# Performance work log

Hardware: AMD Instinct MI355X
Metric: run time of the kernel (lower is better)

The kernel has to match this reference:

```python
import jax, jax.numpy as jnp
import numpy as np
from jax.scipy.linalg import cholesky, solve_triangular

EPS = 0.001

def setup_inputs() -> dict:
    key = jax.random.key(0)
    k1, = jax.random.split(key, 1)
    b, w, h, c = 64, 56, 56, 256
    x = jax.random.normal(k1, (b, w, h, c), dtype=jnp.float32)
    gamma = jnp.ones((c,), dtype=jnp.float32)
    beta = jnp.zeros((c,), dtype=jnp.float32)
    return {"x": x, "gamma": gamma, "beta": beta}

def reference(x, gamma, beta):
    b, w, h, c = x.shape
    n = b * w * h
    # (c, b*w*h) layout as in the original transpose(3,0,1,2)+reshape
    x_flat = jnp.transpose(x, (3, 0, 1, 2)).reshape(c, n)
    m = jnp.mean(x_flat, axis=1, keepdims=True)           # (c, 1)
    f = x_flat - m                                        # (c, n)
    ff = (f @ f.T) / (jnp.float32(n) - 1.0)               # (c, c) covariance
    ff = (1.0 - EPS) * ff + EPS * jnp.eye(c, dtype=x.dtype)
    L = cholesky(ff, lower=True)
    inv_sqrt = solve_triangular(L, jnp.eye(c, dtype=x.dtype), lower=True)  # L^{-1}
    f_hat = inv_sqrt @ f                                  # (c, n) whitened
    out = jnp.transpose(f_hat.reshape(c, b, w, h), (1, 2, 3, 0))
    out = out * gamma.reshape(1, 1, 1, c) + beta.reshape(1, 1, 1, c)
    return out
```

## Files before the change

### kernel.cpp

```cpp
#include <hip/hip_runtime.h>
#include <hip/hip_bf16.h>
#include <math.h>

#define C 256
#define NROWS (64*56*56)
#define EPSV 0.001f
#define TRI(i) (((i)*((i)+1))>>1)

typedef __attribute__((ext_vector_type(8))) short bf16x8;
typedef __attribute__((ext_vector_type(4))) float f32x4;
typedef __attribute__((ext_vector_type(4))) unsigned short u16x4;
typedef __attribute__((ext_vector_type(8))) unsigned short u16x8;
#define MFMA16 __builtin_amdgcn_mfma_f32_16x16x32_bf16

__device__ __forceinline__ int PAD(int i) {
    int a = i >> 2, b = i & 3;
    return ((a + 1) * (2 * a + b)) << 2;
}

__device__ __forceinline__ float bcastf(float v, int l) {
    return __int_as_float(__builtin_amdgcn_readlane(__float_as_int(v), l));
}

__device__ __forceinline__ void split2(float v0, float v1, unsigned& hi, unsigned& lo) {
    unsigned b0 = __float_as_uint(v0), b1 = __float_as_uint(v1);
    hi = (b0 >> 16) | (b1 & 0xFFFF0000u);
    float l0 = v0 - __uint_as_float(b0 & 0xFFFF0000u);
    float l1 = v1 - __uint_as_float(b1 & 0xFFFF0000u);
    lo = (__float_as_uint(l0) >> 16) | (__float_as_uint(l1) & 0xFFFF0000u);
}


template<int W>
__device__ __forceinline__ void cov_step(f32x4* acc, const unsigned* lh, const unsigned* ll,
                                         int m, int kg) {
    constexpr int R0 = W, R1 = 15 - W;
    constexpr int O1 = W + 1;
    bf16x8 ah[2], al[2];
    {
        int r0 = R0 * 16 + m, r1 = R1 * 16 + m;
        int o0 = r0 * 20 + ((kg ^ ((r0 >> 3) & 3)) << 2);
        int o1 = r1 * 20 + ((kg ^ ((r1 >> 3) & 3)) << 2);
        ah[0] = *(const bf16x8*)&lh[o0]; al[0] = *(const bf16x8*)&ll[o0];
        ah[1] = *(const bf16x8*)&lh[o1]; al[1] = *(const bf16x8*)&ll[o1];
    }
#pragma unroll
    for (int c = 0; c <= R1; ++c) {
        int rb = c * 16 + m;
        int ob = rb * 20 + ((kg ^ ((rb >> 3) & 3)) << 2);
        bf16x8 bh = *(const bf16x8*)&lh[ob];
        bf16x8 bl = *(const bf16x8*)&ll[ob];
        if (c <= R0) {
            acc[c] = MFMA16(ah[0], bh, acc[c], 0, 0, 0);
            acc[c] = MFMA16(ah[0], bl, acc[c], 0, 0, 0);
            acc[c] = MFMA16(al[0], bh, acc[c], 0, 0, 0);
        }
        {
            acc[O1 + c] = MFMA16(ah[1], bh, acc[O1 + c], 0, 0, 0);
            acc[O1 + c] = MFMA16(ah[1], bl, acc[O1 + c], 0, 0, 0);
            acc[O1 + c] = MFMA16(al[1], bh, acc[O1 + c], 0, 0, 0);
        }
    }
}

template<int W>
__device__ __forceinline__ void cov_out(const f32x4* acc, float* Sc, int m, int kg) {
    constexpr int R[2] = {W, 15 - W};
    constexpr int O[2] = {0, W + 1};
#pragma unroll
    for (int rr = 0; rr < 2; ++rr) {
        int i0 = R[rr] * 16 + kg * 4;
#pragma unroll
        for (int c = 0; c < 16; ++c) {
            if (c <= R[rr]) {
                int j = c * 16 + m;
#pragma unroll
                for (int q = 0; q < 4; ++q)
                    atomicAdd(&Sc[(i0 + q) * 256 + j], acc[O[rr] + c][q]);
            }
        }
    }
}

__global__ __launch_bounds__(512, 4) void k_cov(const float* __restrict__ x,
                                                float* __restrict__ S8,
                                                float* __restrict__ sums) {
    __shared__ unsigned lh[256 * 20];
    __shared__ unsigned ll_[256 * 20];
    int tid = threadIdx.x, wave = tid >> 6, lane = tid & 63;
    int m = lane & 15, kg = lane >> 4;
    int ch = tid & 255, half = tid >> 8;
    const float* xc = x + (size_t)blockIdx.x * 448 * 256 + ch;
    f32x4 acc[17];
#pragma unroll
    for (int t = 0; t < 17; ++t) acc[t] = 0.f;
    float colsum = 0.f;
    int swkey = (ch >> 3) & 3;

    for (int it = 0; it < 14; ++it) {
        __syncthreads();
        const float* xr = xc + it * 32 * 256;
#pragma unroll
        for (int j = 0; j < 8; ++j) {
            int rp = half * 8 + j;
            float v0 = xr[(2 * rp) * 256];
            float v1 = xr[(2 * rp + 1) * 256];
            colsum += v0 + v1;
            unsigned h, l;
            split2(v0, v1, h, l);
            int idx = ch * 20 + ((((rp >> 2) ^ swkey) << 2) | (rp & 3));
            lh[idx] = h;
            ll_[idx] = l;
        }
        __syncthreads();
        switch (wave) {
            case 0: cov_step<0>(acc, lh, ll_, m, kg); break;
            case 1: cov_step<1>(acc, lh, ll_, m, kg); break;
            case 2: cov_step<2>(acc, lh, ll_, m, kg); break;
            case 3: cov_step<3>(acc, lh, ll_, m, kg); break;
            case 4: cov_step<4>(acc, lh, ll_, m, kg); break;
            case 5: cov_step<5>(acc, lh, ll_, m, kg); break;
            case 6: cov_step<6>(acc, lh, ll_, m, kg); break;
            default: cov_step<7>(acc, lh, ll_, m, kg); break;
        }
    }
    atomicAdd(&sums[ch], colsum);
    float* Sc = S8 + (size_t)(blockIdx.x & 7) * 65536;
    switch (wave) {
        case 0: cov_out<0>(acc, Sc, m, kg); break;
        case 1: cov_out<1>(acc, Sc, m, kg); break;
        case 2: cov_out<2>(acc, Sc, m, kg); break;
        case 3: cov_out<3>(acc, Sc, m, kg); break;
        case 4: cov_out<4>(acc, Sc, m, kg); break;
        case 5: cov_out<5>(acc, Sc, m, kg); break;
        case 6: cov_out<6>(acc, Sc, m, kg); break;
        default: cov_out<7>(acc, Sc, m, kg); break;
    }
}

__global__ __launch_bounds__(256) void k_init(const float* __restrict__ S8,
                                              const float* __restrict__ sums,
                                              float* __restrict__ Lg) {
    int u = blockIdx.x * 256 + threadIdx.x;
    int i = u >> 6, j0 = (u & 63) << 2;
    if (j0 > i) return;
    const float scale = (1.f - EPSV) / ((float)NROWS - 1.f);
    f32x4 s4 = 0.f;
#pragma unroll
    for (int p = 0; p < 8; ++p)
        s4 += *(const f32x4*)&S8[p * 65536 + i * C + j0];
    float mi = sums[i] * (1.f / (float)NROWS);
    f32x4 mj = *(const f32x4*)&sums[j0];
    int base = PAD(i);
#pragma unroll
    for (int e = 0; e < 4; ++e) {
        int j = j0 + e;
        if (j <= i) {
            float v = (s4[e] - mi * mj[e]) * scale;
            if (j == i) v += EPSV;
            Lg[base + j] = v;
        }
    }
}

__global__ __launch_bounds__(512) void k_panel(float* __restrict__ Lg, int kb) {
    __shared__ __align__(16) float DS[32 * 36];
    int tid = threadIdx.x;
    int lane = tid & 63;
    int k0 = kb * 32;

    if (tid < 64) {
        int col = lane & 31;
        float a[32];
#pragma unroll
        for (int i = 0; i < 32; ++i) {
            int ii = (i >= col) ? i : col;
            int jj = (i >= col) ? col : i;
            a[i] = Lg[PAD(k0 + ii) + k0 + jj];
        }
        float drec = 0.f;
#pragma unroll
        for (int k = 0; k < 32; ++k) {
            float akk = bcastf(a[k], k);
            float rinv = rsqrtf(akk);
            float myl = a[k] * rinv;
            bool up = (col > k);
#pragma unroll
            for (int i = k + 1; i < 32; ++i) {
                float lik = bcastf(a[i], k) * rinv;
                if (up) a[i] -= lik * myl;
                if (col == k) a[i] = lik;
            }
            if (col == k) { a[k] = akk * rinv; drec = rinv; }
        }
        float xv[32];
#pragma unroll
        for (int i = 0; i < 32; ++i) xv[i] = (col == i) ? 1.f : 0.f;
#pragma unroll
        for (int i = 0; i < 32; ++i) {
            float di = bcastf(drec, i);
            float xi = xv[i] * di;
            xv[i] = xi;
#pragma unroll
            for (int j = i + 1; j < 32; ++j) {
                float lji = bcastf(a[j], i);
                xv[j] -= lji * xi;
            }
        }
        if (lane < 32) {
#pragma unroll
            for (int i = 0; i < 32; ++i) {
                DS[i * 36 + col] = xv[i];
                if (i >= col) Lg[PAD(k0 + i) + k0 + col] = xv[i];
            }
        }
    }
    __syncthreads();

    int m = 224 - k0;
    int r = tid >> 1, g = tid & 1;
    if (r < m) {
        int abase = PAD(k0 + 32 + r) + k0;
        float4 av[8];
#pragma unroll
        for (int q = 0; q < 8; ++q) av[q] = *(const float4*)&Lg[abase + q * 4];
#pragma unroll
        for (int tgrp = 0; tgrp < 4; ++tgrp) {
            int cbase = g * 16 + tgrp * 4;
            float rv[4];
#pragma unroll
            for (int cc = 0; cc < 4; ++cc) {
                const float* drow = &DS[(cbase + cc) * 36];
                float s = 0.f;
#pragma unroll
                for (int q = 0; q < 8; ++q) {
                    float4 d4 = *(const float4*)&drow[q * 4];
                    s += av[q].x*d4.x + av[q].y*d4.y + av[q].z*d4.z + av[q].w*d4.w;
                }
                rv[cc] = s;
            }
            float4 res; res.x = rv[0]; res.y = rv[1]; res.z = rv[2]; res.w = rv[3];
            *(float4*)&Lg[abase + cbase] = res;
        }
    }
}

__global__ __launch_bounds__(256) void k_trail(float* __restrict__ Lg, int kb) {
    __shared__ __align__(16) float As[32][36];
    __shared__ __align__(16) float Bs[32][36];
    int tid = threadIdx.x;
    int p = blockIdx.x;
    int a2 = 0;
    while (TRI(a2 + 1) <= p) ++a2;
    int b2 = p - TRI(a2);
    int ib2 = kb + 1 + a2, jb2 = kb + 1 + b2;
    int k0 = kb * 32;

    {
        int r = tid >> 3, cq = (tid & 7) * 4;
        *(float4*)&As[r][cq] = *(const float4*)&Lg[PAD(ib2 * 32 + r) + k0 + cq];
        *(float4*)&Bs[r][cq] = *(const float4*)&Lg[PAD(jb2 * 32 + r) + k0 + cq];
    }
    __syncthreads();

    int r2 = (tid >> 4) * 2, c2 = (tid & 15) * 2;
    float t00 = 0, t01 = 0, t10 = 0, t11 = 0;
#pragma unroll 8
    for (int q = 0; q < 32; ++q) {
        float a0 = As[r2][q], a1 = As[r2 + 1][q];
        float b0 = Bs[c2][q], b1 = Bs[c2 + 1][q];
        t00 += a0 * b0; t01 += a0 * b1;
        t10 += a1 * b0; t11 += a1 * b1;
    }
    int gi = ib2 * 32 + r2, gj = jb2 * 32 + c2;
    if (ib2 != jb2) {
        float* p0 = &Lg[PAD(gi) + gj];
        float* p1 = &Lg[PAD(gi + 1) + gj];
        p0[0] -= t00; p0[1] -= t01;
        p1[0] -= t10; p1[1] -= t11;
    } else {
        if (c2     <= r2    ) Lg[PAD(gi) + gj]         -= t00;
        if (c2 + 1 <= r2    ) Lg[PAD(gi) + gj + 1]     -= t01;
        if (c2     <= r2 + 1) Lg[PAD(gi + 1) + gj]     -= t10;
        if (c2 + 1 <= r2 + 1) Lg[PAD(gi + 1) + gj + 1] -= t11;
    }
}

__global__ __launch_bounds__(256) void k_inv(const float* __restrict__ Lg,
                                             const float* __restrict__ sums,
                                             const float* __restrict__ gamma,
                                             unsigned short* __restrict__ Wphi,
                                             unsigned short* __restrict__ Wplo,
                                             float* __restrict__ biasacc) {
    __shared__ __align__(16) float Wcol[256][36];
    __shared__ __align__(16) float Ls[32][36];
    __shared__ __align__(16) float Tst[32][36];
    int jbb = blockIdx.x;
    int tid = threadIdx.x;
    int j0 = jbb * 32;

    {
        int r = tid >> 3, cq = (tid & 7) * 4;
        const float* row = &Lg[PAD(j0 + r) + j0];
        float4 v;
        v.x = (cq     <= r) ? row[cq]     : 0.f;
        v.y = (cq + 1 <= r) ? row[cq + 1] : 0.f;
        v.z = (cq + 2 <= r) ? row[cq + 2] : 0.f;
        v.w = (cq + 3 <= r) ? row[cq + 3] : 0.f;
        *(float4*)&Wcol[j0 + r][cq] = v;
    }
    __syncthreads();

    int r2 = (tid >> 4) * 2, c2 = (tid & 15) * 2;
    for (int ib = jbb + 1; ib < 8; ++ib) {
        int i0 = ib * 32;
        float t00 = 0, t01 = 0, t10 = 0, t11 = 0;
        for (int kb = jbb; kb < ib; ++kb) {
            __syncthreads();
            {
                int r = tid >> 3, cq = (tid & 7) * 4;
                *(float4*)&Ls[r][cq] = *(const float4*)&Lg[PAD(i0 + r) + kb * 32 + cq];
            }
            __syncthreads();
            int kw = kb * 32;
#pragma unroll 8
            for (int q = 0; q < 32; ++q) {
                float l0 = Ls[r2][q], l1 = Ls[r2 + 1][q];
                float w0 = Wcol[kw + q][c2], w1 = Wcol[kw + q][c2 + 1];
                t00 += l0 * w0; t01 += l0 * w1;
                t10 += l1 * w0; t11 += l1 * w1;
            }
        }
        __syncthreads();
        Tst[r2][c2] = t00;     Tst[r2][c2 + 1] = t01;
        Tst[r2 + 1][c2] = t10; Tst[r2 + 1][c2 + 1] = t11;
        {
            int r = tid >> 3, cq = (tid & 7) * 4;
            const float* row = &Lg[PAD(i0 + r) + i0];
            float4 v;
            v.x = (cq     <= r) ? row[cq]     : 0.f;
            v.y = (cq + 1 <= r) ? row[cq + 1] : 0.f;
            v.z = (cq + 2 <= r) ? row[cq + 2] : 0.f;
            v.w = (cq + 3 <= r) ? row[cq + 3] : 0.f;
            *(float4*)&Ls[r][cq] = v;
        }
        __syncthreads();
        float w00 = 0, w01 = 0, w10 = 0, w11 = 0;
#pragma unroll 8
        for (int q = 0; q < 32; ++q) {
            float d0 = Ls[r2][q], d1 = Ls[r2 + 1][q];
            float tq0 = Tst[q][c2], tq1 = Tst[q][c2 + 1];
            w00 += d0 * tq0; w01 += d0 * tq1;
            w10 += d1 * tq0; w11 += d1 * tq1;
        }
        Wcol[i0 + r2][c2] = -w00;     Wcol[i0 + r2][c2 + 1] = -w01;
        Wcol[i0 + r2 + 1][c2] = -w10; Wcol[i0 + r2 + 1][c2 + 1] = -w11;
    }
    __syncthreads();

    {
        int r = tid;
        if (r >= j0) {
            float s = 0.f;
#pragma unroll 8
            for (int c = 0; c < 32; ++c)
                s += Wcol[r][c] * sums[j0 + c];
            atomicAdd(&biasacc[r], s * (1.f / (float)NROWS));
        }
    }
    for (int pi = tid; pi < 1024; pi += 256) {
        int jt = pi >> 6, l = pi & 63;
        int row = jt * 16 + (l & 15);
        int cb = (l >> 4) * 8;
        float g = (row >= j0) ? gamma[row] : 0.f;
        u16x4 h0, h1, lo0, lo1;
#pragma unroll
        for (int j = 0; j < 8; ++j) {
            float v = (row >= j0) ? g * Wcol[row][cb + j] : 0.f;
            unsigned b = __float_as_uint(v);
            unsigned short hi = (unsigned short)(b >> 16);
            float lf = v - __uint_as_float(b & 0xFFFF0000u);
            unsigned short lo = (unsigned short)(__float_as_uint(lf) >> 16);
            if (j < 4) { h0[j] = hi; lo0[j] = lo; }
            else       { h1[j - 4] = hi; lo1[j - 4] = lo; }
        }
        size_t base = ((size_t)(jt * 8 + jbb) * 64 + l) * 8;
        *(u16x4*)&Wphi[base]     = h0;
        *(u16x4*)&Wphi[base + 4] = h1;
        *(u16x4*)&Wplo[base]     = lo0;
        *(u16x4*)&Wplo[base + 4] = lo1;
    }
}

__global__ __launch_bounds__(512) void k_apply(const float* __restrict__ x,
                                               const unsigned short* __restrict__ Wphi,
                                               const unsigned short* __restrict__ Wplo,
                                               const float* __restrict__ beta,
                                               const float* __restrict__ gamma,
                                               const float* __restrict__ biasacc,
                                               float* __restrict__ out) {
    __shared__ unsigned short Bh[8192];
    __shared__ unsigned short Bl[8192];
    int tid = threadIdx.x, wave = tid >> 6, lane = tid & 63;
    int m = lane & 15, kg = lane >> 4;
    size_t rbase = (size_t)blockIdx.x * 128 + wave * 16;
    const float* xr = x + (rbase + m) * 256;

    f32x4 acc[16];
#pragma unroll
    for (int t = 0; t < 16; ++t) acc[t] = 0.f;

#pragma unroll
    for (int kcg = 0; kcg < 8; ++kcg) {
        __syncthreads();
#pragma unroll
        for (int v = tid; v < 1024; v += 512) {
            int jt = v >> 6, off = (v & 63) * 8;
            size_t src = (size_t)(jt * 8 + kcg) * 512 + off;
            int dst = jt * 512 + off;
            *(u16x8*)&Bh[dst] = *(const u16x8*)&Wphi[src];
            *(u16x8*)&Bl[dst] = *(const u16x8*)&Wplo[src];
        }
        f32x4 a0 = *(const f32x4*)&xr[kcg * 32 + kg * 8];
        f32x4 a1 = *(const f32x4*)&xr[kcg * 32 + kg * 8 + 4];
        bf16x8 ah;
#pragma unroll
        for (int e = 0; e < 4; ++e) {
            unsigned b0 = __float_as_uint(a0[e]);
            b0 += 0x7FFFu + ((b0 >> 16) & 1u);
            ah[e] = (short)(b0 >> 16);
            unsigned b1 = __float_as_uint(a1[e]);
            b1 += 0x7FFFu + ((b1 >> 16) & 1u);
            ah[4 + e] = (short)(b1 >> 16);
        }
        __syncthreads();
#pragma unroll
        for (int jt = 0; jt < 16; ++jt) {
            bf16x8 bh = *(const bf16x8*)&Bh[jt * 512 + lane * 8];
            bf16x8 bl = *(const bf16x8*)&Bl[jt * 512 + lane * 8];
            acc[jt] = MFMA16(ah, bh, acc[jt], 0, 0, 0);
            acc[jt] = MFMA16(ah, bl, acc[jt], 0, 0, 0);
        }
    }

#pragma unroll
    for (int jt = 0; jt < 16; ++jt) {
        int j = jt * 16 + m;
        float bb = beta[j] - gamma[j] * biasacc[j];
#pragma unroll
        for (int q = 0; q < 4; ++q)
            out[(rbase + kg * 4 + q) * 256 + j] = acc[jt][q] + bb;
    }
}

extern "C" void kernel_launch(void* const* d_in, const int* in_sizes, int n_in,
                              void* d_out, int out_size, void* d_ws, size_t ws_size,
                              hipStream_t stream) {
    const float* x     = (const float*)d_in[0];
    const float* gamma = (const float*)d_in[1];
    const float* beta  = (const float*)d_in[2];
    float* out  = (float*)d_out;
    float* ws   = (float*)d_ws;
    float* sums     = ws;
    float* biasacc  = ws + 256;
    float* S8       = ws + 512;
    float* Lg       = ws + 524800;
    unsigned short* Wphi = (unsigned short*)(ws + 558080);
    unsigned short* Wplo = (unsigned short*)(ws + 590848);

    hipMemsetAsync(ws, 0, 524800 * sizeof(float), stream);
    hipLaunchKernelGGL(k_cov, dim3(448), dim3(512), 0, stream, x, S8, sums);
    hipLaunchKernelGGL(k_init, dim3(64), dim3(256), 0, stream, S8, sums, Lg);
    for (int kb = 0; kb < 8; ++kb) {
        hipLaunchKernelGGL(k_panel, dim3(1), dim3(512), 0, stream, Lg, kb);
        int np = TRI(7 - kb);
        if (np > 0)
            hipLaunchKernelGGL(k_trail, dim3(np), dim3(256), 0, stream, Lg, kb);
    }
    hipLaunchKernelGGL(k_inv, dim3(8), dim3(256), 0, stream, Lg, sums, gamma, Wphi, Wplo, biasacc);
    hipLaunchKernelGGL(k_apply, dim3(1568), dim3(512), 0, stream, x, Wphi, Wplo, beta, gamma, biasacc, out);
}
```

Measured before the change: 617.7 us.

## Replace atomic covariance reduction with partials and fuse Cholesky into one kernel

The covariance kernel now runs 224 blocks, each covering twice as many rows, and writes its per-wave MFMA accumulators as plain partial tiles instead of issuing atomicAdds into 8 replicated matrices. A new init kernel sums those partials per tile. The 16 separate panel and trailing-update launches are merged into a single-block k_fact kernel that holds the packed lower triangle in LDS for the whole factorization. This removes atomic contention, the large memset and launch overhead, at the cost of fewer cov blocks and a serialized single-workgroup factorization with many barriers.

```diff
diff --git a/kernel.cpp b/kernel.cpp
--- a/kernel.cpp
+++ b/kernel.cpp
@@ -6,6 +6,7 @@
 #define NROWS (64*56*56)
 #define EPSV 0.001f
 #define TRI(i) (((i)*((i)+1))>>1)
+#define NBLK 224
 
 typedef __attribute__((ext_vector_type(8))) short bf16x8;
 typedef __attribute__((ext_vector_type(4))) float f32x4;
@@ -16,10 +17,6 @@
 __device__ __forceinline__ int PAD(int i) {
     int a = i >> 2, b = i & 3;
     return ((a + 1) * (2 * a + b)) << 2;
-}
-
-__device__ __forceinline__ float bcastf(float v, int l) {
-    return __int_as_float(__builtin_amdgcn_readlane(__float_as_int(v), l));
 }
 
 __device__ __forceinline__ void split2(float v0, float v1, unsigned& hi, unsigned& lo) {
@@ -63,41 +60,22 @@
     }
 }
 
-template<int W>
-__device__ __forceinline__ void cov_out(const f32x4* acc, float* Sc, int m, int kg) {
-    constexpr int R[2] = {W, 15 - W};
-    constexpr int O[2] = {0, W + 1};
-#pragma unroll
-    for (int rr = 0; rr < 2; ++rr) {
-        int i0 = R[rr] * 16 + kg * 4;
-#pragma unroll
-        for (int c = 0; c < 16; ++c) {
-            if (c <= R[rr]) {
-                int j = c * 16 + m;
-#pragma unroll
-                for (int q = 0; q < 4; ++q)
-                    atomicAdd(&Sc[(i0 + q) * 256 + j], acc[O[rr] + c][q]);
-            }
-        }
-    }
-}
-
 __global__ __launch_bounds__(512, 4) void k_cov(const float* __restrict__ x,
-                                                float* __restrict__ S8,
+                                                float* __restrict__ P,
                                                 float* __restrict__ sums) {
     __shared__ unsigned lh[256 * 20];
     __shared__ unsigned ll_[256 * 20];
     int tid = threadIdx.x, wave = tid >> 6, lane = tid & 63;
     int m = lane & 15, kg = lane >> 4;
     int ch = tid & 255, half = tid >> 8;
-    const float* xc = x + (size_t)blockIdx.x * 448 * 256 + ch;
+    const float* xc = x + (size_t)blockIdx.x * 896 * 256 + ch;
     f32x4 acc[17];
 #pragma unroll
     for (int t = 0; t < 17; ++t) acc[t] = 0.f;
     float colsum = 0.f;
     int swkey = (ch >> 3) & 3;
 
-    for (int it = 0; it < 14; ++it) {
+    for (int it = 0; it < 28; ++it) {
         __syncthreads();
         const float* xr = xc + it * 32 * 256;
 #pragma unroll
@@ -125,165 +103,208 @@
         }
     }
     atomicAdd(&sums[ch], colsum);
-    float* Sc = S8 + (size_t)(blockIdx.x & 7) * 65536;
-    switch (wave) {
-        case 0: cov_out<0>(acc, Sc, m, kg); break;
-        case 1: cov_out<1>(acc, Sc, m, kg); break;
-        case 2: cov_out<2>(acc, Sc, m, kg); break;
-        case 3: cov_out<3>(acc, Sc, m, kg); break;
-        case 4: cov_out<4>(acc, Sc, m, kg); break;
-        case 5: cov_out<5>(acc, Sc, m, kg); break;
-        case 6: cov_out<6>(acc, Sc, m, kg); break;
-        default: cov_out<7>(acc, Sc, m, kg); break;
-    }
-}
-
-__global__ __launch_bounds__(256) void k_init(const float* __restrict__ S8,
+    float* Pb = P + ((size_t)(blockIdx.x * 8 + wave) * 17) * 256;
+#pragma unroll
+    for (int t = 0; t < 17; ++t)
+        *(f32x4*)&Pb[t * 256 + lane * 4] = acc[t];
+}
+
+__global__ __launch_bounds__(256) void k_init(const float* __restrict__ P,
                                               const float* __restrict__ sums,
                                               float* __restrict__ Lg) {
-    int u = blockIdx.x * 256 + threadIdx.x;
-    int i = u >> 6, j0 = (u & 63) << 2;
-    if (j0 > i) return;
+    int chunk = blockIdx.x;
+    int W = chunk / 17, t = chunk % 17;
+    int R  = (t <= W) ? W : 15 - W;
+    int tj = (t <= W) ? t : t - W - 1;
+    int tid = threadIdx.x;
+    int lane = tid >> 2, q = tid & 3;
+    int kg = lane >> 4, m = lane & 15;
+    int i = R * 16 + kg * 4 + q;
+    int j = tj * 16 + m;
+
+    float s = 0.f;
+    const float* p = P + (size_t)(W * 17 + t) * 256 + tid;
+#pragma unroll 4
+    for (int b = 0; b < NBLK; ++b)
+        s += p[(size_t)b * 8 * 17 * 256];
+
+    if (j > i) return;
     const float scale = (1.f - EPSV) / ((float)NROWS - 1.f);
-    f32x4 s4 = 0.f;
-#pragma unroll
-    for (int p = 0; p < 8; ++p)
-        s4 += *(const f32x4*)&S8[p * 65536 + i * C + j0];
-    float mi = sums[i] * (1.f / (float)NROWS);
-    f32x4 mj = *(const f32x4*)&sums[j0];
-    int base = PAD(i);
-#pragma unroll
-    for (int e = 0; e < 4; ++e) {
-        int j = j0 + e;
-        if (j <= i) {
-            float v = (s4[e] - mi * mj[e]) * scale;
-            if (j == i) v += EPSV;
-            Lg[base + j] = v;
-        }
-    }
-}
-
-__global__ __launch_bounds__(512) void k_panel(float* __restrict__ Lg, int kb) {
-    __shared__ __align__(16) float DS[32 * 36];
+    float v = (s - sums[i] * sums[j] * (1.f / (float)NROWS)) * scale;
+    if (i == j) v += EPSV;
+    Lg[PAD(i) + j] = v;
+}
+
+template<int NR>
+__device__ __forceinline__ void trail_unit(float* __restrict__ Lp, int k0,
+                                           int ib2, int jb2, int r4, int c4) {
+    int gj = jb2 * 32 + c4;
+    int brow[4], arow[NR];
+#pragma unroll
+    for (int cc = 0; cc < 4; ++cc) brow[cc] = PAD(gj + cc) + k0;
+#pragma unroll
+    for (int rr = 0; rr < NR; ++rr) arow[rr] = PAD(ib2 * 32 + r4 + rr) + k0;
+    float acc[NR][4];
+#pragma unroll
+    for (int rr = 0; rr < NR; ++rr)
+#pragma unroll
+        for (int cc = 0; cc < 4; ++cc) acc[rr][cc] = 0.f;
+#pragma unroll
+    for (int k4 = 0; k4 < 32; k4 += 4) {
+        float4 b0 = *(const float4*)&Lp[brow[0] + k4];
+        float4 b1 = *(const float4*)&Lp[brow[1] + k4];
+        float4 b2 = *(const float4*)&Lp[brow[2] + k4];
+        float4 b3 = *(const float4*)&Lp[brow[3] + k4];
+#pragma unroll
+        for (int rr = 0; rr < NR; ++rr) {
+            float4 av = *(const float4*)&Lp[arow[rr] + k4];
+            acc[rr][0] += av.x*b0.x + av.y*b0.y + av.z*b0.z + av.w*b0.w;
+            acc[rr][1] += av.x*b1.x + av.y*b1.y + av.z*b1.z + av.w*b1.w;
+            acc[rr][2] += av.x*b2.x + av.y*b2.y + av.z*b2.z + av.w*b2.w;
+            acc[rr][3] += av.x*b3.x + av.y*b3.y + av.z*b3.z + av.w*b3.w;
+        }
+    }
+    if (ib2 != jb2) {
+#pragma unroll
+        for (int rr = 0; rr < NR; ++rr) {
+            int wb = PAD(ib2 * 32 + r4 + rr) + gj;
+            float4 o = *(const float4*)&Lp[wb];
+            o.x -= acc[rr][0]; o.y -= acc[rr][1]; o.z -= acc[rr][2]; o.w -= acc[rr][3];
+            *(float4*)&Lp[wb] = o;
+        }
+    } else {
+#pragma unroll
+        for (int rr = 0; rr < NR; ++rr) {
+            int rloc = r4 + rr;
+            int wb = PAD(ib2 * 32 + rloc) + gj;
+#pragma unroll
+            for (int cc = 0; cc < 4; ++cc)
+                if (c4 + cc <= rloc) Lp[wb + cc] -= acc[rr][cc];
+        }
+    }
+}
+
+__global__ __launch_bounds__(512, 2) void k_fact(float* __restrict__ Lg) {
+    __shared__ __align__(16) float Lp[33280];
+    __shared__ __align__(16) float D0[1056];
+    __shared__ __align__(16) float DS[1152];
     int tid = threadIdx.x;
-    int lane = tid & 63;
-    int k0 = kb * 32;
-
-    if (tid < 64) {
-        int col = lane & 31;
-        float a[32];
-#pragma unroll
-        for (int i = 0; i < 32; ++i) {
-            int ii = (i >= col) ? i : col;
-            int jj = (i >= col) ? col : i;
-            a[i] = Lg[PAD(k0 + ii) + k0 + jj];
-        }
-        float drec = 0.f;
-#pragma unroll
+    int slot = tid >> 6, sub = tid & 63;
+    int c4 = (sub & 7) * 4;
+
+    for (int u = tid; u < 8320; u += 512)
+        *(f32x4*)&Lp[u * 4] = *(const f32x4*)&Lg[u * 4];
+
+    int ei0, ej0, ei1 = -1, ej1 = 0;
+    {
+        int e = tid;
+        int i = (int)((sqrtf(8.f * (float)e + 1.f) - 1.f) * 0.5f);
+        while (TRI(i) > e) --i;
+        while (TRI(i + 1) <= e) ++i;
+        ei0 = i; ej0 = e - TRI(i);
+        if (tid + 512 < 528) { ei1 = 31; ej1 = tid + 512 - TRI(31); }
+    }
+    __syncthreads();
+
+    for (int kb = 0; kb < 8; ++kb) {
+        int k0 = kb * 32;
+        D0[ei0 * 33 + ej0] = Lp[PAD(k0 + ei0) + k0 + ej0];
+        if (ei1 >= 0) D0[ei1 * 33 + ej1] = Lp[PAD(k0 + ei1) + k0 + ej1];
+        for (int u = tid; u < 1152; u += 512) DS[u] = 0.f;
+        __syncthreads();
+
         for (int k = 0; k < 32; ++k) {
-            float akk = bcastf(a[k], k);
-            float rinv = rsqrtf(akk);
-            float myl = a[k] * rinv;
-            bool up = (col > k);
-#pragma unroll
-            for (int i = k + 1; i < 32; ++i) {
-                float lik = bcastf(a[i], k) * rinv;
-                if (up) a[i] -= lik * myl;
-                if (col == k) a[i] = lik;
-            }
-            if (col == k) { a[k] = akk * rinv; drec = rinv; }
-        }
-        float xv[32];
-#pragma unroll
-        for (int i = 0; i < 32; ++i) xv[i] = (col == i) ? 1.f : 0.f;
-#pragma unroll
-        for (int i = 0; i < 32; ++i) {
-            float di = bcastf(drec, i);
-            float xi = xv[i] * di;
-            xv[i] = xi;
-#pragma unroll
-            for (int j = i + 1; j < 32; ++j) {
-                float lji = bcastf(a[j], i);
-                xv[j] -= lji * xi;
-            }
-        }
-        if (lane < 32) {
-#pragma unroll
-            for (int i = 0; i < 32; ++i) {
-                DS[i * 36 + col] = xv[i];
-                if (i >= col) Lg[PAD(k0 + i) + k0 + col] = xv[i];
-            }
-        }
-    }
-    __syncthreads();
-
-    int m = 224 - k0;
-    int r = tid >> 1, g = tid & 1;
-    if (r < m) {
-        int abase = PAD(k0 + 32 + r) + k0;
-        float4 av[8];
-#pragma unroll
-        for (int q = 0; q < 8; ++q) av[q] = *(const float4*)&Lg[abase + q * 4];
-#pragma unroll
-        for (int tgrp = 0; tgrp < 4; ++tgrp) {
-            int cbase = g * 16 + tgrp * 4;
-            float rv[4];
-#pragma unroll
-            for (int cc = 0; cc < 4; ++cc) {
-                const float* drow = &DS[(cbase + cc) * 36];
+            float rinv = 1.f / D0[k * 33 + k];
+            bool a0 = (ej0 > k);
+            bool a1 = (ei1 >= 0) && (ej1 > k);
+            if (a0) D0[ei0 * 33 + ej0] -= D0[ei0 * 33 + k] * D0[ej0 * 33 + k] * rinv;
+            if (a1) D0[ei1 * 33 + ej1] -= D0[ei1 * 33 + k] * D0[ej1 * 33 + k] * rinv;
+            __syncthreads();
+        }
+        {
+            float s0 = D0[ej0 * 33 + ej0];
+            float s1 = (ei1 >= 0) ? D0[ej1 * 33 + ej1] : 1.f;
+            __syncthreads();
+            if (ei0 > ej0) D0[ei0 * 33 + ej0] *= rsqrtf(s0);
+            else           D0[ei0 * 33 + ei0]  = sqrtf(s0);
+            if (ei1 >= 0) {
+                if (ei1 > ej1) D0[ei1 * 33 + ej1] *= rsqrtf(s1);
+                else           D0[ei1 * 33 + ei1]  = sqrtf(s1);
+            }
+            __syncthreads();
+        }
+        if (tid < 32) {
+            int c = tid;
+            float xi = 1.f / D0[c * 33 + c];
+            DS[c * 36 + c] = xi;
+            Lp[PAD(k0 + c) + k0 + c] = xi;
+            for (int i2 = c + 1; i2 < 32; ++i2) {
                 float s = 0.f;
-#pragma unroll
-                for (int q = 0; q < 8; ++q) {
-                    float4 d4 = *(const float4*)&drow[q * 4];
-                    s += av[q].x*d4.x + av[q].y*d4.y + av[q].z*d4.z + av[q].w*d4.w;
+                for (int k = c; k < i2; ++k)
+                    s += D0[i2 * 33 + k] * DS[k * 36 + c];
+                float v = -s / D0[i2 * 33 + i2];
+                DS[i2 * 36 + c] = v;
+                Lp[PAD(k0 + i2) + k0 + c] = v;
+            }
+        }
+        __syncthreads();
+
+        {
+            int mrows = 224 - k0;
+            int r = tid >> 1, g = tid & 1;
+            if (r < mrows) {
+                int abase = PAD(k0 + 32 + r) + k0;
+                float4 av[8];
+#pragma unroll
+                for (int q = 0; q < 8; ++q) av[q] = *(const float4*)&Lp[abase + q * 4];
+#pragma unroll
+                for (int tgrp = 0; tgrp < 4; ++tgrp) {
+                    int cbase = g * 16 + tgrp * 4;
+                    float rv[4];
+#pragma unroll
+                    for (int cc = 0; cc < 4; ++cc) {
+                        const float* drow = &DS[(cbase + cc) * 36];
+                        float s = 0.f;
+#pragma unroll
+                        for (int q = 0; q < 8; ++q) {
+                            float4 d4 = *(const float4*)&drow[q * 4];
+                            s += av[q].x*d4.x + av[q].y*d4.y + av[q].z*d4.z + av[q].w*d4.w;
+                        }
+                        rv[cc] = s;
+                    }
+                    float4 res; res.x = rv[0]; res.y = rv[1]; res.z = rv[2]; res.w = rv[3];
+                    *(float4*)&Lp[abase + cbase] = res;
                 }
-                rv[cc] = s;
-            }
-            float4 res; res.x = rv[0]; res.y = rv[1]; res.z = rv[2]; res.w = rv[3];
-            *(float4*)&Lg[abase + cbase] = res;
-        }
-    }
-}
-
-__global__ __launch_bounds__(256) void k_trail(float* __restrict__ Lg, int kb) {
-    __shared__ __align__(16) float As[32][36];
-    __shared__ __align__(16) float Bs[32][36];
-    int tid = threadIdx.x;
-    int p = blockIdx.x;
-    int a2 = 0;
-    while (TRI(a2 + 1) <= p) ++a2;
-    int b2 = p - TRI(a2);
-    int ib2 = kb + 1 + a2, jb2 = kb + 1 + b2;
-    int k0 = kb * 32;
-
-    {
-        int r = tid >> 3, cq = (tid & 7) * 4;
-        *(float4*)&As[r][cq] = *(const float4*)&Lg[PAD(ib2 * 32 + r) + k0 + cq];
-        *(float4*)&Bs[r][cq] = *(const float4*)&Lg[PAD(jb2 * 32 + r) + k0 + cq];
-    }
-    __syncthreads();
-
-    int r2 = (tid >> 4) * 2, c2 = (tid & 15) * 2;
-    float t00 = 0, t01 = 0, t10 = 0, t11 = 0;
-#pragma unroll 8
-    for (int q = 0; q < 32; ++q) {
-        float a0 = As[r2][q], a1 = As[r2 + 1][q];
-        float b0 = Bs[c2][q], b1 = Bs[c2 + 1][q];
-        t00 += a0 * b0; t01 += a0 * b1;
-        t10 += a1 * b0; t11 += a1 * b1;
-    }
-    int gi = ib2 * 32 + r2, gj = jb2 * 32 + c2;
-    if (ib2 != jb2) {
-        float* p0 = &Lg[PAD(gi) + gj];
-        float* p1 = &Lg[PAD(gi + 1) + gj];
-        p0[0] -= t00; p0[1] -= t01;
-        p1[0] -= t10; p1[1] -= t11;
-    } else {
-        if (c2     <= r2    ) Lg[PAD(gi) + gj]         -= t00;
-        if (c2 + 1 <= r2    ) Lg[PAD(gi) + gj + 1]     -= t01;
-        if (c2     <= r2 + 1) Lg[PAD(gi + 1) + gj]     -= t10;
-        if (c2 + 1 <= r2 + 1) Lg[PAD(gi + 1) + gj + 1] -= t11;
-    }
+            }
+        }
+        __syncthreads();
+
+        {
+            int npairs = TRI(7 - kb);
+            if (npairs > 0) {
+                int lsp = (npairs >= 8) ? 0 : (npairs >= 3 ? 1 : 2);
+                int splitR = 1 << lsp;
+                int units = npairs << lsp;
+                int rows_pu = 32 >> lsp;
+                for (int u = slot; u < units; u += 8) {
+                    int p = u >> lsp, rpart = u & (splitR - 1);
+                    int a2 = 0;
+                    while (TRI(a2 + 1) <= p) ++a2;
+                    int b2 = p - TRI(a2);
+                    int ib2 = kb + 1 + a2, jb2 = kb + 1 + b2;
+                    int nrq = rows_pu >> 3;
+                    int r4 = rpart * rows_pu + (sub >> 3) * nrq;
+                    if (lsp == 0)      trail_unit<4>(Lp, k0, ib2, jb2, r4, c4);
+                    else if (lsp == 1) trail_unit<2>(Lp, k0, ib2, jb2, r4, c4);
+                    else               trail_unit<1>(Lp, k0, ib2, jb2, r4, c4);
+                }
+            }
+        }
+        __syncthreads();
+    }
+
+    for (int u = tid; u < 8320; u += 512)
+        *(f32x4*)&Lg[u * 4] = *(const f32x4*)&Lp[u * 4];
 }
 
 __global__ __launch_bounds__(256) void k_inv(const float* __restrict__ Lg,
@@ -463,20 +484,15 @@
     float* ws   = (float*)d_ws;
     float* sums     = ws;
     float* biasacc  = ws + 256;
-    float* S8       = ws + 512;
-    float* Lg       = ws + 524800;
-    unsigned short* Wphi = (unsigned short*)(ws + 558080);
-    unsigned short* Wplo = (unsigned short*)(ws + 590848);
-
-    hipMemsetAsync(ws, 0, 524800 * sizeof(float), stream);
-    hipLaunchKernelGGL(k_cov, dim3(448), dim3(512), 0, stream, x, S8, sums);
-    hipLaunchKernelGGL(k_init, dim3(64), dim3(256), 0, stream, S8, sums, Lg);
-    for (int kb = 0; kb < 8; ++kb) {
-        hipLaunchKernelGGL(k_panel, dim3(1), dim3(512), 0, stream, Lg, kb);
-        int np = TRI(7 - kb);
-        if (np > 0)
-            hipLaunchKernelGGL(k_trail, dim3(np), dim3(256), 0, stream, Lg, kb);
-    }
+    float* Lg       = ws + 512;
+    float* P        = ws + 33792;
+    unsigned short* Wphi = (unsigned short*)(ws + 7832576);
+    unsigned short* Wplo = (unsigned short*)(ws + 7865344);
+
+    hipMemsetAsync(ws, 0, 512 * sizeof(float), stream);
+    hipLaunchKernelGGL(k_cov, dim3(NBLK), dim3(512), 0, stream, x, P, sums);
+    hipLaunchKernelGGL(k_init, dim3(136), dim3(256), 0, stream, P, sums, Lg);
+    hipLaunchKernelGGL(k_fact, dim3(1), dim3(512), 0, stream, Lg);
     hipLaunchKernelGGL(k_inv, dim3(8), dim3(256), 0, stream, Lg, sums, gamma, Wphi, Wplo, biasacc);
     hipLaunchKernelGGL(k_apply, dim3(1568), dim3(512), 0, stream, x, Wphi, Wplo, beta, gamma, biasacc, out);
 }
```

Result: faster. 579.8 us (-6.1%).

## Fuse Cholesky, inverse and reduction into one cooperative kernel

Applied to the files above, without the earlier changes.

The covariance kernel now writes per-wave partial accumulators to a workspace instead of doing atomic adds into eight copies. It also uses half as many blocks, each covering twice as many rows. A single cooperative kernel with 28 blocks reduces the partials, builds the padded lower triangle, runs the blocked Cholesky panel and trailing updates separated by grid syncs, and computes the inverse. This removes about 17 small launches and the atomic traffic. The cost is a larger partial buffer, a serial reduction over 224 blocks, grid-sync overhead, and lower parallelism in the covariance pass.

```diff
diff --git a/kernel.cpp b/kernel.cpp
--- a/kernel.cpp
+++ b/kernel.cpp
@@ -1,11 +1,15 @@
 #include <hip/hip_runtime.h>
 #include <hip/hip_bf16.h>
+#include <hip/hip_cooperative_groups.h>
 #include <math.h>
+
+namespace cg = cooperative_groups;
 
 #define C 256
 #define NROWS (64*56*56)
 #define EPSV 0.001f
 #define TRI(i) (((i)*((i)+1))>>1)
+#define NBLK 224
 
 typedef __attribute__((ext_vector_type(8))) short bf16x8;
 typedef __attribute__((ext_vector_type(4))) float f32x4;
@@ -63,41 +67,22 @@
     }
 }
 
-template<int W>
-__device__ __forceinline__ void cov_out(const f32x4* acc, float* Sc, int m, int kg) {
-    constexpr int R[2] = {W, 15 - W};
-    constexpr int O[2] = {0, W + 1};
-#pragma unroll
-    for (int rr = 0; rr < 2; ++rr) {
-        int i0 = R[rr] * 16 + kg * 4;
-#pragma unroll
-        for (int c = 0; c < 16; ++c) {
-            if (c <= R[rr]) {
-                int j = c * 16 + m;
-#pragma unroll
-                for (int q = 0; q < 4; ++q)
-                    atomicAdd(&Sc[(i0 + q) * 256 + j], acc[O[rr] + c][q]);
-            }
-        }
-    }
-}
-
 __global__ __launch_bounds__(512, 4) void k_cov(const float* __restrict__ x,
-                                                float* __restrict__ S8,
+                                                float* __restrict__ P,
                                                 float* __restrict__ sums) {
     __shared__ unsigned lh[256 * 20];
     __shared__ unsigned ll_[256 * 20];
     int tid = threadIdx.x, wave = tid >> 6, lane = tid & 63;
     int m = lane & 15, kg = lane >> 4;
     int ch = tid & 255, half = tid >> 8;
-    const float* xc = x + (size_t)blockIdx.x * 448 * 256 + ch;
+    const float* xc = x + (size_t)blockIdx.x * 896 * 256 + ch;
     f32x4 acc[17];
 #pragma unroll
     for (int t = 0; t < 17; ++t) acc[t] = 0.f;
     float colsum = 0.f;
     int swkey = (ch >> 3) & 3;
 
-    for (int it = 0; it < 14; ++it) {
+    for (int it = 0; it < 28; ++it) {
         __syncthreads();
         const float* xr = xc + it * 32 * 256;
 #pragma unroll
@@ -125,270 +110,282 @@
         }
     }
     atomicAdd(&sums[ch], colsum);
-    float* Sc = S8 + (size_t)(blockIdx.x & 7) * 65536;
-    switch (wave) {
-        case 0: cov_out<0>(acc, Sc, m, kg); break;
-        case 1: cov_out<1>(acc, Sc, m, kg); break;
-        case 2: cov_out<2>(acc, Sc, m, kg); break;
-        case 3: cov_out<3>(acc, Sc, m, kg); break;
-        case 4: cov_out<4>(acc, Sc, m, kg); break;
-        case 5: cov_out<5>(acc, Sc, m, kg); break;
-        case 6: cov_out<6>(acc, Sc, m, kg); break;
-        default: cov_out<7>(acc, Sc, m, kg); break;
-    }
-}
-
-__global__ __launch_bounds__(256) void k_init(const float* __restrict__ S8,
-                                              const float* __restrict__ sums,
-                                              float* __restrict__ Lg) {
-    int u = blockIdx.x * 256 + threadIdx.x;
-    int i = u >> 6, j0 = (u & 63) << 2;
-    if (j0 > i) return;
-    const float scale = (1.f - EPSV) / ((float)NROWS - 1.f);
-    f32x4 s4 = 0.f;
-#pragma unroll
-    for (int p = 0; p < 8; ++p)
-        s4 += *(const f32x4*)&S8[p * 65536 + i * C + j0];
-    float mi = sums[i] * (1.f / (float)NROWS);
-    f32x4 mj = *(const f32x4*)&sums[j0];
-    int base = PAD(i);
-#pragma unroll
-    for (int e = 0; e < 4; ++e) {
-        int j = j0 + e;
-        if (j <= i) {
-            float v = (s4[e] - mi * mj[e]) * scale;
-            if (j == i) v += EPSV;
-            Lg[base + j] = v;
-        }
-    }
-}
-
-__global__ __launch_bounds__(512) void k_panel(float* __restrict__ Lg, int kb) {
-    __shared__ __align__(16) float DS[32 * 36];
-    int tid = threadIdx.x;
-    int lane = tid & 63;
-    int k0 = kb * 32;
-
-    if (tid < 64) {
-        int col = lane & 31;
-        float a[32];
-#pragma unroll
-        for (int i = 0; i < 32; ++i) {
-            int ii = (i >= col) ? i : col;
-            int jj = (i >= col) ? col : i;
-            a[i] = Lg[PAD(k0 + ii) + k0 + jj];
-        }
-        float drec = 0.f;
-#pragma unroll
-        for (int k = 0; k < 32; ++k) {
-            float akk = bcastf(a[k], k);
-            float rinv = rsqrtf(akk);
-            float myl = a[k] * rinv;
-            bool up = (col > k);
-#pragma unroll
-            for (int i = k + 1; i < 32; ++i) {
-                float lik = bcastf(a[i], k) * rinv;
-                if (up) a[i] -= lik * myl;
-                if (col == k) a[i] = lik;
-            }
-            if (col == k) { a[k] = akk * rinv; drec = rinv; }
-        }
-        float xv[32];
-#pragma unroll
-        for (int i = 0; i < 32; ++i) xv[i] = (col == i) ? 1.f : 0.f;
-#pragma unroll
-        for (int i = 0; i < 32; ++i) {
-            float di = bcastf(drec, i);
-            float xi = xv[i] * di;
-            xv[i] = xi;
-#pragma unroll
-            for (int j = i + 1; j < 32; ++j) {
-                float lji = bcastf(a[j], i);
-                xv[j] -= lji * xi;
-            }
-        }
-        if (lane < 32) {
-#pragma unroll
-            for (int i = 0; i < 32; ++i) {
-                DS[i * 36 + col] = xv[i];
-                if (i >= col) Lg[PAD(k0 + i) + k0 + col] = xv[i];
-            }
-        }
-    }
-    __syncthreads();
-
-    int m = 224 - k0;
-    int r = tid >> 1, g = tid & 1;
-    if (r < m) {
-        int abase = PAD(k0 + 32 + r) + k0;
-        float4 av[8];
-#pragma unroll
-        for (int q = 0; q < 8; ++q) av[q] = *(const float4*)&Lg[abase + q * 4];
-#pragma unroll
-        for (int tgrp = 0; tgrp < 4; ++tgrp) {
-            int cbase = g * 16 + tgrp * 4;
-            float rv[4];
-#pragma unroll
-            for (int cc = 0; cc < 4; ++cc) {
-                const float* drow = &DS[(cbase + cc) * 36];
-                float s = 0.f;
-#pragma unroll
-                for (int q = 0; q < 8; ++q) {
-                    float4 d4 = *(const float4*)&drow[q * 4];
-                    s += av[q].x*d4.x + av[q].y*d4.y + av[q].z*d4.z + av[q].w*d4.w;
-                }
-                rv[cc] = s;
-            }
-            float4 res; res.x = rv[0]; res.y = rv[1]; res.z = rv[2]; res.w = rv[3];
-            *(float4*)&Lg[abase + cbase] = res;
-        }
-    }
-}
-
-__global__ __launch_bounds__(256) void k_trail(float* __restrict__ Lg, int kb) {
+    float* Pb = P + ((size_t)(blockIdx.x * 8 + wave) * 17) * 256;
+#pragma unroll
+    for (int t = 0; t < 17; ++t)
+        *(f32x4*)&Pb[t * 256 + lane * 4] = acc[t];
+}
+
+__device__ __attribute__((noinline)) void diag_fact(float* __restrict__ Lg, int k0, int tid) {
+    if (tid >= 64) return;
+    int col = tid & 31;
+    float a[32];
+#pragma unroll
+    for (int i = 0; i < 32; ++i) {
+        int ii = (i >= col) ? i : col;
+        int jj = (i >= col) ? col : i;
+        a[i] = Lg[PAD(k0 + ii) + k0 + jj];
+    }
+    float drec = 0.f;
+#pragma unroll
+    for (int k = 0; k < 32; ++k) {
+        float akk = bcastf(a[k], k);
+        float rinv = rsqrtf(akk);
+        float myl = a[k] * rinv;
+        bool up = (col > k);
+#pragma unroll
+        for (int i = k + 1; i < 32; ++i) {
+            float lik = bcastf(a[i], k) * rinv;
+            if (up) a[i] -= lik * myl;
+            if (col == k) a[i] = lik;
+        }
+        if (col == k) { a[k] = akk * rinv; drec = rinv; }
+    }
+    float xv[32];
+#pragma unroll
+    for (int i = 0; i < 32; ++i) xv[i] = (col == i) ? 1.f : 0.f;
+#pragma unroll
+    for (int i = 0; i < 32; ++i) {
+        float di = bcastf(drec, i);
+        float xi = xv[i] * di;
+        xv[i] = xi;
+#pragma unroll
+        for (int j = i + 1; j < 32; ++j) {
+            float lji = bcastf(a[j], i);
+            xv[j] -= lji * xi;
+        }
+    }
+    if (tid < 32) {
+#pragma unroll
+        for (int i = 0; i < 32; ++i)
+            if (i >= col) Lg[PAD(k0 + i) + k0 + col] = xv[i];
+    }
+}
+
+__global__ __launch_bounds__(256) void k_factco(const float* __restrict__ P,
+                                                const float* __restrict__ sums,
+                                                const float* __restrict__ gamma,
+                                                float* __restrict__ Lg,
+                                                unsigned short* __restrict__ Wphi,
+                                                unsigned short* __restrict__ Wplo,
+                                                float* __restrict__ biasacc) {
+    cg::grid_group grid = cg::this_grid();
+    __shared__ __align__(16) float DS[1152];
     __shared__ __align__(16) float As[32][36];
     __shared__ __align__(16) float Bs[32][36];
-    int tid = threadIdx.x;
-    int p = blockIdx.x;
-    int a2 = 0;
-    while (TRI(a2 + 1) <= p) ++a2;
-    int b2 = p - TRI(a2);
-    int ib2 = kb + 1 + a2, jb2 = kb + 1 + b2;
-    int k0 = kb * 32;
-
-    {
-        int r = tid >> 3, cq = (tid & 7) * 4;
-        *(float4*)&As[r][cq] = *(const float4*)&Lg[PAD(ib2 * 32 + r) + k0 + cq];
-        *(float4*)&Bs[r][cq] = *(const float4*)&Lg[PAD(jb2 * 32 + r) + k0 + cq];
-    }
-    __syncthreads();
-
-    int r2 = (tid >> 4) * 2, c2 = (tid & 15) * 2;
-    float t00 = 0, t01 = 0, t10 = 0, t11 = 0;
-#pragma unroll 8
-    for (int q = 0; q < 32; ++q) {
-        float a0 = As[r2][q], a1 = As[r2 + 1][q];
-        float b0 = Bs[c2][q], b1 = Bs[c2 + 1][q];
-        t00 += a0 * b0; t01 += a0 * b1;
-        t10 += a1 * b0; t11 += a1 * b1;
-    }
-    int gi = ib2 * 32 + r2, gj = jb2 * 32 + c2;
-    if (ib2 != jb2) {
-        float* p0 = &Lg[PAD(gi) + gj];
-        float* p1 = &Lg[PAD(gi + 1) + gj];
-        p0[0] -= t00; p0[1] -= t01;
-        p1[0] -= t10; p1[1] -= t11;
-    } else {
-        if (c2     <= r2    ) Lg[PAD(gi) + gj]         -= t00;
-        if (c2 + 1 <= r2    ) Lg[PAD(gi) + gj + 1]     -= t01;
-        if (c2     <= r2 + 1) Lg[PAD(gi + 1) + gj]     -= t10;
-        if (c2 + 1 <= r2 + 1) Lg[PAD(gi + 1) + gj + 1] -= t11;
-    }
-}
-
-__global__ __launch_bounds__(256) void k_inv(const float* __restrict__ Lg,
-                                             const float* __restrict__ sums,
-                                             const float* __restrict__ gamma,
-                                             unsigned short* __restrict__ Wphi,
-                                             unsigned short* __restrict__ Wplo,
-                                             float* __restrict__ biasacc) {
     __shared__ __align__(16) float Wcol[256][36];
     __shared__ __align__(16) float Ls[32][36];
     __shared__ __align__(16) float Tst[32][36];
-    int jbb = blockIdx.x;
-    int tid = threadIdx.x;
-    int j0 = jbb * 32;
-
-    {
-        int r = tid >> 3, cq = (tid & 7) * 4;
-        const float* row = &Lg[PAD(j0 + r) + j0];
-        float4 v;
-        v.x = (cq     <= r) ? row[cq]     : 0.f;
-        v.y = (cq + 1 <= r) ? row[cq + 1] : 0.f;
-        v.z = (cq + 2 <= r) ? row[cq + 2] : 0.f;
-        v.w = (cq + 3 <= r) ? row[cq + 3] : 0.f;
-        *(float4*)&Wcol[j0 + r][cq] = v;
-    }
-    __syncthreads();
-
-    int r2 = (tid >> 4) * 2, c2 = (tid & 15) * 2;
-    for (int ib = jbb + 1; ib < 8; ++ib) {
-        int i0 = ib * 32;
-        float t00 = 0, t01 = 0, t10 = 0, t11 = 0;
-        for (int kb = jbb; kb < ib; ++kb) {
-            __syncthreads();
-            {
-                int r = tid >> 3, cq = (tid & 7) * 4;
-                *(float4*)&Ls[r][cq] = *(const float4*)&Lg[PAD(i0 + r) + kb * 32 + cq];
-            }
-            __syncthreads();
-            int kw = kb * 32;
-#pragma unroll 8
-            for (int q = 0; q < 32; ++q) {
-                float l0 = Ls[r2][q], l1 = Ls[r2 + 1][q];
-                float w0 = Wcol[kw + q][c2], w1 = Wcol[kw + q][c2 + 1];
-                t00 += l0 * w0; t01 += l0 * w1;
-                t10 += l1 * w0; t11 += l1 * w1;
-            }
-        }
-        __syncthreads();
-        Tst[r2][c2] = t00;     Tst[r2][c2 + 1] = t01;
-        Tst[r2 + 1][c2] = t10; Tst[r2 + 1][c2 + 1] = t11;
+    int tid = threadIdx.x, bid = blockIdx.x;
+
+    for (int chunk = bid; chunk < 136; chunk += 28) {
+        int W = chunk / 17, t = chunk % 17;
+        int R  = (t <= W) ? W : 15 - W;
+        int tj = (t <= W) ? t : t - W - 1;
+        int lane = tid >> 2, q = tid & 3;
+        int kg = lane >> 4, m = lane & 15;
+        int i = R * 16 + kg * 4 + q;
+        int j = tj * 16 + m;
+        float s = 0.f;
+        const float* p = P + (size_t)chunk * 256 + tid;
+#pragma unroll 4
+        for (int b = 0; b < NBLK; ++b)
+            s += p[(size_t)b * 8 * 17 * 256];
+        if (j <= i) {
+            const float scale = (1.f - EPSV) / ((float)NROWS - 1.f);
+            float v = (s - sums[i] * sums[j] * (1.f / (float)NROWS)) * scale;
+            if (i == j) v += EPSV;
+            Lg[PAD(i) + j] = v;
+        }
+    }
+    grid.sync();
+
+    if (bid == 0) diag_fact(Lg, 0, tid);
+    grid.sync();
+
+    for (int kb = 0; kb < 7; ++kb) {
+        int k0 = kb * 32;
+
         {
             int r = tid >> 3, cq = (tid & 7) * 4;
-            const float* row = &Lg[PAD(i0 + r) + i0];
+            const float* row = &Lg[PAD(k0 + r) + k0];
             float4 v;
             v.x = (cq     <= r) ? row[cq]     : 0.f;
             v.y = (cq + 1 <= r) ? row[cq + 1] : 0.f;
             v.z = (cq + 2 <= r) ? row[cq + 2] : 0.f;
             v.w = (cq + 3 <= r) ? row[cq + 3] : 0.f;
-            *(float4*)&Ls[r][cq] = v;
-        }
-        __syncthreads();
-        float w00 = 0, w01 = 0, w10 = 0, w11 = 0;
+            *(float4*)&DS[r * 36 + cq] = v;
+        }
+        __syncthreads();
+        {
+            int mrows = 224 - k0;
+            int rl = tid >> 1, g = tid & 1;
+            int r = bid * 8 + rl;
+            if (rl < 8 && r < mrows) {
+                int abase = PAD(k0 + 32 + r) + k0;
+                float4 av[8];
+#pragma unroll
+                for (int q = 0; q < 8; ++q) av[q] = *(const float4*)&Lg[abase + q * 4];
+#pragma unroll
+                for (int tgrp = 0; tgrp < 4; ++tgrp) {
+                    int cbase = g * 16 + tgrp * 4;
+                    float rv[4];
+#pragma unroll
+                    for (int cc = 0; cc < 4; ++cc) {
+                        const float* drow = &DS[(cbase + cc) * 36];
+                        float s = 0.f;
+#pragma unroll
+                        for (int q = 0; q < 8; ++q) {
+                            float4 d4 = *(const float4*)&drow[q * 4];
+                            s += av[q].x*d4.x + av[q].y*d4.y + av[q].z*d4.z + av[q].w*d4.w;
+                        }
+                        rv[cc] = s;
+                    }
+                    float4 res; res.x = rv[0]; res.y = rv[1]; res.z = rv[2]; res.w = rv[3];
+                    *(float4*)&Lg[abase + cbase] = res;
+                }
+            }
+        }
+        grid.sync();
+
+        {
+            int npairs = TRI(7 - kb);
+            if (bid < npairs) {
+                int p = bid;
+                int a2 = 0;
+                while (TRI(a2 + 1) <= p) ++a2;
+                int b2 = p - TRI(a2);
+                int ib2 = kb + 1 + a2, jb2 = kb + 1 + b2;
+                {
+                    int r = tid >> 3, cq = (tid & 7) * 4;
+                    *(float4*)&As[r][cq] = *(const float4*)&Lg[PAD(ib2 * 32 + r) + k0 + cq];
+                    *(float4*)&Bs[r][cq] = *(const float4*)&Lg[PAD(jb2 * 32 + r) + k0 + cq];
+                }
+                __syncthreads();
+                int r2 = (tid >> 4) * 2, c2 = (tid & 15) * 2;
+                float t00 = 0, t01 = 0, t10 = 0, t11 = 0;
 #pragma unroll 8
-        for (int q = 0; q < 32; ++q) {
-            float d0 = Ls[r2][q], d1 = Ls[r2 + 1][q];
-            float tq0 = Tst[q][c2], tq1 = Tst[q][c2 + 1];
-            w00 += d0 * tq0; w01 += d0 * tq1;
-            w10 += d1 * tq0; w11 += d1 * tq1;
-        }
-        Wcol[i0 + r2][c2] = -w00;     Wcol[i0 + r2][c2 + 1] = -w01;
-        Wcol[i0 + r2 + 1][c2] = -w10; Wcol[i0 + r2 + 1][c2 + 1] = -w11;
-    }
-    __syncthreads();
-
-    {
-        int r = tid;
-        if (r >= j0) {
-            float s = 0.f;
+                for (int q = 0; q < 32; ++q) {
+                    float a0 = As[r2][q], a1 = As[r2 + 1][q];
+                    float b0 = Bs[c2][q], b1 = Bs[c2 + 1][q];
+                    t00 += a0 * b0; t01 += a0 * b1;
+                    t10 += a1 * b0; t11 += a1 * b1;
+                }
+                int gi = ib2 * 32 + r2, gj = jb2 * 32 + c2;
+                if (ib2 != jb2) {
+                    float* p0 = &Lg[PAD(gi) + gj];
+                    float* p1 = &Lg[PAD(gi + 1) + gj];
+                    p0[0] -= t00; p0[1] -= t01;
+                    p1[0] -= t10; p1[1] -= t11;
+                } else {
+                    if (c2     <= r2    ) Lg[PAD(gi) + gj]         -= t00;
+                    if (c2 + 1 <= r2    ) Lg[PAD(gi) + gj + 1]     -= t01;
+                    if (c2     <= r2 + 1) Lg[PAD(gi + 1) + gj]     -= t10;
+                    if (c2 + 1 <= r2 + 1) Lg[PAD(gi + 1) + gj + 1] -= t11;
+                }
+                if (bid == 0) {
+                    __syncthreads();
+                    diag_fact(Lg, (kb + 1) * 32, tid);
+                }
+            }
+        }
+        grid.sync();
+    }
+
+    if (bid < 8) {
+        int jbb = bid;
+        int j0 = jbb * 32;
+        {
+            int r = tid >> 3, cq = (tid & 7) * 4;
+            const float* row = &Lg[PAD(j0 + r) + j0];
+            float4 v;
+            v.x = (cq     <= r) ? row[cq]     : 0.f;
+            v.y = (cq + 1 <= r) ? row[cq + 1] : 0.f;
+            v.z = (cq + 2 <= r) ? row[cq + 2] : 0.f;
+            v.w = (cq + 3 <= r) ? row[cq + 3] : 0.f;
+            *(float4*)&Wcol[j0 + r][cq] = v;
+        }
+        __syncthreads();
+
+        int r2 = (tid >> 4) * 2, c2 = (tid & 15) * 2;
+        for (int ib = jbb + 1; ib < 8; ++ib) {
+            int i0 = ib * 32;
+            float t00 = 0, t01 = 0, t10 = 0, t11 = 0;
+            for (int kb = jbb; kb < ib; ++kb) {
+                __syncthreads();
+                {
+                    int r = tid >> 3, cq = (tid & 7) * 4;
+                    *(float4*)&Ls[r][cq] = *(const float4*)&Lg[PAD(i0 + r) + kb * 32 + cq];
+                }
+                __syncthreads();
+                int kw = kb * 32;
 #pragma unroll 8
-            for (int c = 0; c < 32; ++c)
-                s += Wcol[r][c] * sums[j0 + c];
-            atomicAdd(&biasacc[r], s * (1.f / (float)NROWS));
-        }
-    }
-    for (int pi = tid; pi < 1024; pi += 256) {
-        int jt = pi >> 6, l = pi & 63;
-        int row = jt * 16 + (l & 15);
-        int cb = (l >> 4) * 8;
-        float g = (row >= j0) ? gamma[row] : 0.f;
-        u16x4 h0, h1, lo0, lo1;
-#pragma unroll
-        for (int j = 0; j < 8; ++j) {
-            float v = (row >= j0) ? g * Wcol[row][cb + j] : 0.f;
-            unsigned b = __float_as_uint(v);
-            unsigned short hi = (unsigned short)(b >> 16);
-            float lf = v - __uint_as_float(b & 0xFFFF0000u);
-            unsigned short lo = (unsigned short)(__float_as_uint(lf) >> 16);
-            if (j < 4) { h0[j] = hi; lo0[j] = lo; }
-            else       { h1[j - 4] = hi; lo1[j - 4] = lo; }
-        }
-        size_t base = ((size_t)(jt * 8 + jbb) * 64 + l) * 8;
-        *(u16x4*)&Wphi[base]     = h0;
-        *(u16x4*)&Wphi[base + 4] = h1;
-        *(u16x4*)&Wplo[base]     = lo0;
-        *(u16x4*)&Wplo[base + 4] = lo1;
+                for (int q = 0; q < 32; ++q) {
+                    float l0 = Ls[r2][q], l1 = Ls[r2 + 1][q];
+                    float w0 = Wcol[kw + q][c2], w1 = Wcol[kw + q][c2 + 1];
+                    t00 += l0 * w0; t01 += l0 * w1;
+                    t10 += l1 * w0; t11 += l1 * w1;
+                }
+            }
+            __syncthreads();
+            Tst[r2][c2] = t00;     Tst[r2][c2 + 1] = t01;
+            Tst[r2 + 1][c2] = t10; Tst[r2 + 1][c2 + 1] = t11;
+            {
+                int r = tid >> 3, cq = (tid & 7) * 4;
+                const float* row = &Lg[PAD(i0 + r) + i0];
+                float4 v;
+                v.x = (cq     <= r) ? row[cq]     : 0.f;
+                v.y = (cq + 1 <= r) ? row[cq + 1] : 0.f;
+                v.z = (cq + 2 <= r) ? row[cq + 2] : 0.f;
+                v.w = (cq + 3 <= r) ? row[cq + 3] : 0.f;
+                *(float4*)&Ls[r][cq] = v;
+            }
+            __syncthreads();
+            float w00 = 0, w01 = 0, w10 = 0, w11 = 0;
+#pragma unroll 8
+            for (int q = 0; q < 32; ++q) {
+                float d0 = Ls[r2][q], d1 = Ls[r2 + 1][q];
+                float tq0 = Tst[q][c2], tq1 = Tst[q][c2 + 1];
+                w00 += d0 * tq0; w01 += d0 * tq1;
+                w10 += d1 * tq0; w11 += d1 * tq1;
+            }
+            Wcol[i0 + r2][c2] = -w00;     Wcol[i0 + r2][c2 + 1] = -w01;
+            Wcol[i0 + r2 + 1][c2] = -w10; Wcol[i0 + r2 + 1][c2 + 1] = -w11;
+        }
+        __syncthreads();
+
+        {
+            int r = tid;
+            if (r >= j0) {
+                float s = 0.f;
+#pragma unroll 8
+                for (int c = 0; c < 32; ++c)
+                    s += Wcol[r][c] * sums[j0 + c];
+                atomicAdd(&biasacc[r], s * (1.f / (float)NROWS));
+            }
+        }
+        for (int pi = tid; pi < 1024; pi += 256) {
+            int jt = pi >> 6, l = pi & 63;
+            int row = jt * 16 + (l & 15);
+            int cb = (l >> 4) * 8;
+            float g = (row >= j0) ? gamma[row] : 0.f;
+            u16x4 h0, h1, lo0, lo1;
+#pragma unroll
+            for (int j = 0; j < 8; ++j) {
+                float v = (row >= j0) ? g * Wcol[row][cb + j] : 0.f;
+                unsigned b = __float_as_uint(v);
+                unsigned short hi = (unsigned short)(b >> 16);
+                float lf = v - __uint_as_float(b & 0xFFFF0000u);
+                unsigned short lo = (unsigned short)(__float_as_uint(lf) >> 16);
+                if (j < 4) { h0[j] = hi; lo0[j] = lo; }
+                else       { h1[j - 4] = hi; lo1[j - 4] = lo; }
+            }
+            size_t base = ((size_t)(jt * 8 + jbb) * 64 + l) * 8;
+            *(u16x4*)&Wphi[base]     = h0;
+            *(u16x4*)&Wphi[base + 4] = h1;
+            *(u16x4*)&Wplo[base]     = lo0;
+            *(u16x4*)&Wplo[base + 4] = lo1;
+        }
     }
 }
 
@@ -463,20 +460,18 @@
     float* ws   = (float*)d_ws;
     float* sums     = ws;
     float* biasacc  = ws + 256;
-    float* S8       = ws + 512;
-    float* Lg       = ws + 524800;
-    unsigned short* Wphi = (unsigned short*)(ws + 558080);
-    unsigned short* Wplo = (unsigned short*)(ws + 590848);
-
-    hipMemsetAsync(ws, 0, 524800 * sizeof(float), stream);
-    hipLaunchKernelGGL(k_cov, dim3(448), dim3(512), 0, stream, x, S8, sums);
-    hipLaunchKernelGGL(k_init, dim3(64), dim3(256), 0, stream, S8, sums, Lg);
-    for (int kb = 0; kb < 8; ++kb) {
-        hipLaunchKernelGGL(k_panel, dim3(1), dim3(512), 0, stream, Lg, kb);
-        int np = TRI(7 - kb);
-        if (np > 0)
-            hipLaunchKernelGGL(k_trail, dim3(np), dim3(256), 0, stream, Lg, kb);
-    }
-    hipLaunchKernelGGL(k_inv, dim3(8), dim3(256), 0, stream, Lg, sums, gamma, Wphi, Wplo, biasacc);
+    float* Lg       = ws + 512;
+    float* P        = ws + 33792;
+    unsigned short* Wphi = (unsigned short*)(ws + 7832576);
+    unsigned short* Wplo = (unsigned short*)(ws + 7865344);
+
+    hipMemsetAsync(ws, 0, 512 * sizeof(float), stream);
+    hipLaunchKernelGGL(k_cov, dim3(NBLK), dim3(512), 0, stream, x, P, sums);
+    {
+        void* args[] = { (void*)&P, (void*)&sums, (void*)&gamma, (void*)&Lg,
+                         (void*)&Wphi, (void*)&Wplo, (void*)&biasacc };
+        hipLaunchCooperativeKernel((const void*)k_factco, dim3(28), dim3(256),
+                                   args, 0, stream);
+    }
     hipLaunchKernelGGL(k_apply, dim3(1568), dim3(512), 0, stream, x, Wphi, Wplo, beta, gamma, biasacc, out);
 }
```

Result: slower. 667.2 us (+8.0%).
